# Optimization experiments

Hardware: AMD Instinct MI355X
Metric: run time of the kernel (lower is better)

Reference implementation:

```python
import jax, jax.numpy as jnp
import numpy as np

G = 32            # gridsize
N = G * G         # num_nodes = 1024
F_IN = 32         # input_dim
H = 256           # hidden_dim
L = 4             # n_layers
B = 64            # batch
MID = F_IN + L * H
MIN_VAL = -10000000.0
EPS_LN = 1e-5
EPS_BN = 1e-5


def _grid_edges():
    ids = np.arange(N).reshape(G, G)
    hs, hd = ids[:, :-1].ravel(), ids[:, 1:].ravel()
    vs, vd = ids[:-1, :].ravel(), ids[1:, :].ravel()
    src = np.concatenate([hs, hd, vs, vd]).astype(np.int32)
    dst = np.concatenate([hd, hs, vd, vs]).astype(np.int32)
    return jnp.asarray(src), jnp.asarray(dst)


def setup_inputs() -> dict:
    key = jax.random.key(0)
    ks = jax.random.split(key, 16)
    mask_f = jax.random.bernoulli(ks[0], 0.7, (B, N)).astype(jnp.float32)
    feats = jax.random.normal(ks[1], (B, N * F_IN), dtype=jnp.float32)
    observations = jnp.concatenate([mask_f, feats], axis=1)
    src, dst = _grid_edges()
    def lin(k, fi, fo):
        return jax.random.normal(k, (fi, fo), dtype=jnp.float32) / np.sqrt(fi)
    W0 = lin(ks[2], F_IN, H); b0 = jnp.zeros((H,), jnp.float32)
    g0 = jnp.ones((H,), jnp.float32); be0 = jnp.zeros((H,), jnp.float32)
    Ws = jax.random.normal(ks[3], (L - 1, H, H), jnp.float32) / np.sqrt(H)
    bs = jnp.zeros((L - 1, H), jnp.float32)
    gs = jnp.ones((L - 1, H), jnp.float32); bes = jnp.zeros((L - 1, H), jnp.float32)
    W1 = lin(ks[4], MID, 2 * H); b1 = jnp.zeros((2 * H,), jnp.float32)
    bn_g = jnp.ones((2 * H,), jnp.float32); bn_b = jnp.zeros((2 * H,), jnp.float32)
    bn_m = jax.random.normal(ks[5], (2 * H,), jnp.float32) * 0.1
    bn_v = jax.random.uniform(ks[6], (2 * H,), jnp.float32, 0.5, 1.5)
    W2 = lin(ks[7], 2 * H, 1); b2 = jnp.zeros((1,), jnp.float32)
    return {"observations": observations, "src": src, "dst": dst,
            "W0": W0, "b0": b0, "g0": g0, "be0": be0,
            "Ws": Ws, "bs": bs, "gs": gs, "bes": bes,
            "W1": W1, "b1": b1, "bn_g": bn_g, "bn_b": bn_b,
            "bn_m": bn_m, "bn_v": bn_v, "W2": W2, "b2": b2}


def _layer_norm(z, g, b):
    mu = z.mean(-1, keepdims=True)
    var = z.var(-1, keepdims=True)
    return (z - mu) / jnp.sqrt(var + EPS_LN) * g + b


def reference(observations, src, dst, W0, b0, g0, be0, Ws, bs, gs, bes,
              W1, b1, bn_g, bn_b, bn_m, bn_v, W2, b2):
    mask = observations[:, :N] != 0.0                      # [B,N] bool action mask
    x = observations[:, N:].reshape(B, N, F_IN)            # node features
    outs = [x]
    h = x
    for l in range(L):
        # GIN with eps=-1: (1+eps)*x_i vanishes -> mlp(sum of neighbor features)
        agg = jnp.zeros_like(h).at[:, dst, :].add(h[:, src, :])
        W, bb, g, be = ((W0, b0, g0, be0) if l == 0
                        else (Ws[l - 1], bs[l - 1], gs[l - 1], bes[l - 1]))
        h = jax.nn.relu(_layer_norm(agg @ W + bb, g, be))  # mlp ReLU; outer .relu() is idempotent
        outs.append(h)
    xc = jnp.concatenate(outs, axis=-1).reshape(B * N, MID)
    z = xc @ W1 + b1
    z = (z - bn_m) / jnp.sqrt(bn_v + EPS_BN) * bn_g + bn_b  # BatchNorm1d eval mode
    z = jax.nn.relu(z)                                       # dropout off in eval
    y = (z @ W2 + b2).reshape(B, N)
    return jnp.where(mask, y, MIN_VAL)
```

## Files before the change

### kernel.cpp

```cpp
#include <hip/hip_runtime.h>
#include <stdint.h>

#define FIN 32
#define HD 256
#define MIDK 1056
#define HF 512
#define MROWS 65536
#define OBS_STRIDE 33792

typedef float f32x2 __attribute__((ext_vector_type(2)));
typedef float f32x4 __attribute__((ext_vector_type(4)));

__device__ __forceinline__ unsigned pack4fp8(float a, float b, float c, float d) {
    int w = __builtin_amdgcn_cvt_pk_fp8_f32(a, b, 0, false);
    return (unsigned)__builtin_amdgcn_cvt_pk_fp8_f32(c, d, w, true);
}
__device__ __forceinline__ unsigned char f2fp8(float f) {
    return (unsigned char)(__builtin_amdgcn_cvt_pk_fp8_f32(f, f, 0, false) & 0xff);
}

__device__ __forceinline__ void glds16(const void* g, void* l) {
    __builtin_amdgcn_global_load_lds(
        (const __attribute__((address_space(1))) unsigned int*)g,
        (__attribute__((address_space(3))) unsigned int*)l,
        16, 0, 0);
}

__device__ __forceinline__ void gather16(const float* __restrict__ src, int stride, int n,
                                         unsigned char* __restrict__ dst) {
    float f[16];
#pragma unroll
    for (int j = 0; j < 16; ++j) f[j] = src[(size_t)j * stride + n];
    uint4 o;
    o.x = pack4fp8(f[0],  f[1],  f[2],  f[3]);
    o.y = pack4fp8(f[4],  f[5],  f[6],  f[7]);
    o.z = pack4fp8(f[8],  f[9],  f[10], f[11]);
    o.w = pack4fp8(f[12], f[13], f[14], f[15]);
    *(uint4*)dst = o;
}

__global__ __launch_bounds__(256) void k_prep_w(
        const float* __restrict__ W0, const float* __restrict__ Ws,
        const float* __restrict__ W1,
        unsigned char* __restrict__ Wt0, unsigned char* __restrict__ WtL,
        unsigned char* __restrict__ WtF) {
    const int b = blockIdx.x, t = threadIdx.x;
    if (b < 2) {
        int s = b * 256 + t;
        int hh = s >> 8, n = s & 255;
        gather16(W0 + (size_t)(hh * 16) * HD, HD, n, Wt0 + (size_t)s * 16);
    } else if (b < 50) {
        int u = (b - 2) * 256 + t;
        int l = u >> 12, s = u & 4095;
        int kb = s >> 9, hh = (s >> 8) & 1, n = s & 255;
        gather16(Ws + (size_t)l * 65536 + (size_t)(kb * 32 + hh * 16) * HD, HD, n,
                 WtL + (size_t)l * 65536 + (size_t)s * 16);
    } else {
        int s = (b - 50) * 256 + t;
        int kb = s >> 11, hh = (s >> 9) & 3, n = s & 511;
        int k0 = kb * 64 + hh * 16;
        if (k0 < MIDK)
            gather16(W1 + (size_t)k0 * HF, HF, n, WtF + (size_t)s * 16);
        else
            *(uint4*)(WtF + (size_t)s * 16) = make_uint4(0, 0, 0, 0);
    }
}

template <int K>
__global__ __launch_bounds__(256, 4) void k_layer(
        const unsigned char* __restrict__ Hin,
        const float* __restrict__ obs,
        const unsigned char* __restrict__ Wt,
        const float* __restrict__ bias, const float* __restrict__ gamma,
        const float* __restrict__ beta, unsigned char* __restrict__ Hout) {
    constexpr int KB = K / 32;
    __shared__ __align__(16) unsigned char Agg[(K / 16) * 64 * 16];
    __shared__ float ls[64], lss[64];
    const int t = threadIdx.x;
    const int w = t >> 6, lane = t & 63, quad = lane >> 4, l15 = lane & 15;
    const int q1 = quad >> 1, q0 = quad & 1;
    const int m0 = ((blockIdx.x & 7) * 128 + (blockIdx.x >> 3)) * 64;
    if (t < 64) { ls[t] = 0.f; lss[t] = 0.f; }

    if constexpr (K == 256) {
        const int r32 = t >> 3, seg = t & 7;
        const size_t rowBase = (size_t)(m0 & ~1023);
#pragma unroll
        for (int p = 0; p < 2; ++p) {
            const int r = p * 32 + r32;
            const int node = (m0 + r) & 1023;
            const int rr = node >> 5, cc = node & 31;
            float s[32];
#pragma unroll
            for (int i = 0; i < 32; ++i) s[i] = 0.f;
            auto addn = [&](int nn) {
                const uint4* pp = (const uint4*)(Hin + (rowBase + nn) * (size_t)K + seg * 32);
                uint4 u0 = pp[0], u1 = pp[1];
                unsigned uu[8] = {u0.x, u0.y, u0.z, u0.w, u1.x, u1.y, u1.z, u1.w};
#pragma unroll
                for (int i = 0; i < 8; ++i) {
                    f32x2 lo = __builtin_amdgcn_cvt_pk_f32_fp8(uu[i], false);
                    f32x2 hi = __builtin_amdgcn_cvt_pk_f32_fp8(uu[i], true);
                    s[4 * i + 0] += lo.x; s[4 * i + 1] += lo.y;
                    s[4 * i + 2] += hi.x; s[4 * i + 3] += hi.y;
                }
            };
            if (cc > 0)  addn(node - 1);
            if (cc < 31) addn(node + 1);
            if (rr > 0)  addn(node - 32);
            if (rr < 31) addn(node + 32);
            unsigned ow[8];
#pragma unroll
            for (int i = 0; i < 8; ++i)
                ow[i] = pack4fp8(s[4 * i], s[4 * i + 1], s[4 * i + 2], s[4 * i + 3]);
            ((uint4*)Agg)[(2 * seg) * 64 + r]     = make_uint4(ow[0], ow[1], ow[2], ow[3]);
            ((uint4*)Agg)[(2 * seg + 1) * 64 + r] = make_uint4(ow[4], ow[5], ow[6], ow[7]);
        }
    } else {
        const int r = t >> 2, seg4 = t & 3;
        const int bimg = m0 >> 10;
        const int node = (m0 + r) & 1023;
        const int rr = node >> 5, cc = node & 31;
        const float* fb = obs + (size_t)bimg * OBS_STRIDE + 1024 + seg4 * 8;
        float s[8] = {0, 0, 0, 0, 0, 0, 0, 0};
        auto addnf = [&](int nn) {
            const float4* fp = (const float4*)(fb + nn * 32);
            float4 f0 = fp[0], f1 = fp[1];
            s[0] += f0.x; s[1] += f0.y; s[2] += f0.z; s[3] += f0.w;
            s[4] += f1.x; s[5] += f1.y; s[6] += f1.z; s[7] += f1.w;
        };
        if (cc > 0)  addnf(node - 1);
        if (cc < 31) addnf(node + 1);
        if (rr > 0)  addnf(node - 32);
        if (rr < 31) addnf(node + 32);
        uint2 o;
        o.x = pack4fp8(s[0], s[1], s[2], s[3]);
        o.y = pack4fp8(s[4], s[5], s[6], s[7]);
        *(uint2*)(Agg + ((seg4 >> 1) * 64 + r) * 16 + (seg4 & 1) * 8) = o;
    }
    __syncthreads();

    f32x4 acc[4][4] = {};
    const unsigned char* bbase = Wt + ((size_t)(q1 * 256 + w * 64 + l15)) * 16 + q0 * 8;
    const unsigned char* abase = Agg + ((size_t)(q1 * 64 + l15)) * 16 + q0 * 8;

#define LOADBL(dst, kb) { const unsigned char* bp = bbase + (size_t)(kb) * 8192; \
    dst[0] = *(const long long*)(bp);        dst[1] = *(const long long*)(bp + 256); \
    dst[2] = *(const long long*)(bp + 512);  dst[3] = *(const long long*)(bp + 768); }
#define MFMAL(buf, kb) { long long af[4]; \
    _Pragma("unroll") for (int mt = 0; mt < 4; ++mt) \
        af[mt] = *(const long long*)(abase + (kb) * 2048 + mt * 256); \
    _Pragma("unroll") for (int mt = 0; mt < 4; ++mt) \
    _Pragma("unroll") for (int nt = 0; nt < 4; ++nt) \
        acc[mt][nt] = __builtin_amdgcn_mfma_f32_16x16x32_fp8_fp8(af[mt], buf[nt], acc[mt][nt], 0, 0, 0); }

    if constexpr (KB == 1) {
        long long bA[4];
        LOADBL(bA, 0);
        MFMAL(bA, 0);
    } else {
        long long bA[4], bB[4];
        LOADBL(bA, 0);
#pragma unroll
        for (int j = 0; j < KB / 2 - 1; ++j) {
            LOADBL(bB, 2 * j + 1);
            MFMAL(bA, 2 * j);
            LOADBL(bA, 2 * j + 2);
            MFMAL(bB, 2 * j + 1);
        }
        LOADBL(bB, KB - 1);
        MFMAL(bA, KB - 2);
        MFMAL(bB, KB - 1);
    }
#undef LOADBL
#undef MFMAL

#pragma unroll
    for (int mt = 0; mt < 4; ++mt) {
        float s0 = 0, s1 = 0, s2 = 0, s3 = 0, u0 = 0, u1 = 0, u2 = 0, u3 = 0;
#pragma unroll
        for (int nt = 0; nt < 4; ++nt) {
            int col = w * 64 + nt * 16 + l15;
            float bv = bias[col];
            f32x4 vv = acc[mt][nt];
            vv.x += bv; vv.y += bv; vv.z += bv; vv.w += bv;
            acc[mt][nt] = vv;
            s0 += vv.x; u0 += vv.x * vv.x;
            s1 += vv.y; u1 += vv.y * vv.y;
            s2 += vv.z; u2 += vv.z * vv.z;
            s3 += vv.w; u3 += vv.w * vv.w;
        }
#pragma unroll
        for (int msk = 1; msk < 16; msk <<= 1) {
            s0 += __shfl_xor(s0, msk); u0 += __shfl_xor(u0, msk);
            s1 += __shfl_xor(s1, msk); u1 += __shfl_xor(u1, msk);
            s2 += __shfl_xor(s2, msk); u2 += __shfl_xor(u2, msk);
            s3 += __shfl_xor(s3, msk); u3 += __shfl_xor(u3, msk);
        }
        if (l15 == 0) {
            int rl = mt * 16 + quad * 4;
            atomicAdd(&ls[rl + 0], s0); atomicAdd(&lss[rl + 0], u0);
            atomicAdd(&ls[rl + 1], s1); atomicAdd(&lss[rl + 1], u1);
            atomicAdd(&ls[rl + 2], s2); atomicAdd(&lss[rl + 2], u2);
            atomicAdd(&ls[rl + 3], s3); atomicAdd(&lss[rl + 3], u3);
        }
    }
    __syncthreads();
#pragma unroll
    for (int mt = 0; mt < 4; ++mt) {
        int rl = mt * 16 + quad * 4;
        float mu0 = ls[rl + 0] * (1.f / 256.f), mu1 = ls[rl + 1] * (1.f / 256.f);
        float mu2 = ls[rl + 2] * (1.f / 256.f), mu3 = ls[rl + 3] * (1.f / 256.f);
        float rs0 = rsqrtf(lss[rl + 0] * (1.f / 256.f) - mu0 * mu0 + 1e-5f);
        float rs1 = rsqrtf(lss[rl + 1] * (1.f / 256.f) - mu1 * mu1 + 1e-5f);
        float rs2 = rsqrtf(lss[rl + 2] * (1.f / 256.f) - mu2 * mu2 + 1e-5f);
        float rs3 = rsqrtf(lss[rl + 3] * (1.f / 256.f) - mu3 * mu3 + 1e-5f);
#pragma unroll
        for (int nt = 0; nt < 4; ++nt) {
            int col = w * 64 + nt * 16 + l15;
            float gg = gamma[col], be = beta[col];
            f32x4 vv = acc[mt][nt];
            size_t rb = (size_t)(m0 + mt * 16 + quad * 4) * HD + col;
            Hout[rb]          = f2fp8(fmaxf((vv.x - mu0) * rs0 * gg + be, 0.f));
            Hout[rb + HD]     = f2fp8(fmaxf((vv.y - mu1) * rs1 * gg + be, 0.f));
            Hout[rb + 2 * HD] = f2fp8(fmaxf((vv.z - mu2) * rs2 * gg + be, 0.f));
            Hout[rb + 3 * HD] = f2fp8(fmaxf((vv.w - mu3) * rs3 * gg + be, 0.f));
        }
    }
}

__global__ __launch_bounds__(512) void k_final(
        const unsigned char* __restrict__ h0, const unsigned char* __restrict__ h1,
        const unsigned char* __restrict__ h2, const unsigned char* __restrict__ h3,
        const unsigned char* __restrict__ WtF,
        const float* __restrict__ b1,
        const float* __restrict__ bng, const float* __restrict__ bnb,
        const float* __restrict__ bnm, const float* __restrict__ bnv,
        const float* __restrict__ W2, const float* __restrict__ b2,
        const float* __restrict__ obs, float* __restrict__ out) {
    __shared__ __align__(16) unsigned char As[264 * 16];
    __shared__ __align__(16) unsigned char Bsm[2056 * 16];
    __shared__ float yred[64];
    const int t = threadIdx.x;
    const int w = t >> 6, lane = t & 63, quad = lane >> 4, l15 = lane & 15;
    const int q1 = quad >> 1, q0 = quad & 1;
    const int wr = w >> 2, wc = w & 3;
    const int m0 = ((blockIdx.x & 7) * 128 + (blockIdx.x >> 3)) * 64;
    const int bimg = m0 >> 10, node0 = m0 & 1023;
    if (t < 64) yred[t] = 0.f;

    const unsigned char* hbuf[4] = {h0, h1, h2, h3};
    f32x4 acc[2][8] = {};

    for (int iter = 0; iter < 17; ++iter) {
        const int kb = iter * 64;
        const int steps = (iter < 16) ? 2 : 1;
        if (iter == 0) {
            if (t < 128) {
                int h = t >> 6, r = t & 63;
                const float* p = obs + (size_t)bimg * OBS_STRIDE + 1024 + (node0 + r) * 32 + h * 16;
                float4 f0 = *(const float4*)p, f1 = *(const float4*)(p + 4);
                float4 f2 = *(const float4*)(p + 8), f3 = *(const float4*)(p + 12);
                uint4 o;
                o.x = pack4fp8(f0.x, f0.y, f0.z, f0.w);
                o.y = pack4fp8(f1.x, f1.y, f1.z, f1.w);
                o.z = pack4fp8(f2.x, f2.y, f2.z, f2.w);
                o.w = pack4fp8(f3.x, f3.y, f3.z, f3.w);
                *(uint4*)(As + (h * 66 + r) * 16) = o;
            } else if (t < 256) {
                int h = t >> 6;
                glds16(h0 + (size_t)(m0 + (t & 63)) * HD + (h - 2) * 16,
                       As + (size_t)h * 66 * 16);
            }
        } else if (t < steps * 128) {
            int h = t >> 6, r = t & 63;
            int j = kb + h * 16 - FIN;
            glds16(hbuf[j >> 8] + (size_t)(m0 + r) * HD + (j & 255),
                   As + (size_t)h * 66 * 16);
        }
        for (int i = 0; i < steps * 2; ++i)
            glds16(WtF + ((size_t)iter * 2048 + i * 512 + t) * 16,
                   Bsm + ((size_t)i * 514 + (t & ~63)) * 16);
        __syncthreads();
#pragma unroll 2
        for (int s2 = 0; s2 < steps; ++s2) {
            long long af[2], bf[8];
#pragma unroll
            for (int mt = 0; mt < 2; ++mt)
                af[mt] = *(const long long*)(As + ((s2 * 2 + q1) * 66 + wr * 32 + mt * 16 + l15) * 16 + q0 * 8);
#pragma unroll
            for (int nt = 0; nt < 8; ++nt)
                bf[nt] = *(const long long*)(Bsm + ((size_t)((s2 * 2 + q1) * 514 + wc * 128 + nt * 16 + l15)) * 16 + q0 * 8);
#pragma unroll
            for (int mt = 0; mt < 2; ++mt)
#pragma unroll
                for (int nt = 0; nt < 8; ++nt)
                    acc[mt][nt] = __builtin_amdgcn_mfma_f32_16x16x32_fp8_fp8(af[mt], bf[nt], acc[mt][nt], 0, 0, 0);
        }
        __syncthreads();
    }

    float scv[8], sbv[8], w2v[8];
#pragma unroll
    for (int nt = 0; nt < 8; ++nt) {
        int col = wc * 128 + nt * 16 + l15;
        float sc = bng[col] * rsqrtf(bnv[col] + 1e-5f);
        scv[nt] = sc;
        sbv[nt] = (b1[col] - bnm[col]) * sc + bnb[col];
        w2v[nt] = W2[col];
    }
#pragma unroll
    for (int mt = 0; mt < 2; ++mt) {
        float p0 = 0, p1 = 0, p2 = 0, p3 = 0;
#pragma unroll
        for (int nt = 0; nt < 8; ++nt) {
            f32x4 vv = acc[mt][nt];
            p0 += fmaxf(vv.x * scv[nt] + sbv[nt], 0.f) * w2v[nt];
            p1 += fmaxf(vv.y * scv[nt] + sbv[nt], 0.f) * w2v[nt];
            p2 += fmaxf(vv.z * scv[nt] + sbv[nt], 0.f) * w2v[nt];
            p3 += fmaxf(vv.w * scv[nt] + sbv[nt], 0.f) * w2v[nt];
        }
#pragma unroll
        for (int msk = 1; msk < 16; msk <<= 1) {
            p0 += __shfl_xor(p0, msk);
            p1 += __shfl_xor(p1, msk);
            p2 += __shfl_xor(p2, msk);
            p3 += __shfl_xor(p3, msk);
        }
        if (l15 == 0) {
            int rl = wr * 32 + mt * 16 + quad * 4;
            atomicAdd(&yred[rl + 0], p0);
            atomicAdd(&yred[rl + 1], p1);
            atomicAdd(&yred[rl + 2], p2);
            atomicAdd(&yred[rl + 3], p3);
        }
    }
    __syncthreads();
    if (t < 64) {
        int gm = m0 + t;
        float mk = obs[(size_t)bimg * OBS_STRIDE + (node0 + t)];
        out[gm] = (mk != 0.f) ? yred[t] + b2[0] : -10000000.0f;
    }
}

extern "C" void kernel_launch(void* const* d_in, const int* in_sizes, int n_in,
                              void* d_out, int out_size, void* d_ws, size_t ws_size,
                              hipStream_t stream) {
    const float* obs = (const float*)d_in[0];
    const float* W0  = (const float*)d_in[3];
    const float* b0  = (const float*)d_in[4];
    const float* g0  = (const float*)d_in[5];
    const float* be0 = (const float*)d_in[6];
    const float* Ws  = (const float*)d_in[7];
    const float* bs  = (const float*)d_in[8];
    const float* gs  = (const float*)d_in[9];
    const float* bes = (const float*)d_in[10];
    const float* W1  = (const float*)d_in[11];
    const float* b1  = (const float*)d_in[12];
    const float* bng = (const float*)d_in[13];
    const float* bnb = (const float*)d_in[14];
    const float* bnm = (const float*)d_in[15];
    const float* bnv = (const float*)d_in[16];
    const float* W2  = (const float*)d_in[17];
    const float* b2  = (const float*)d_in[18];
    float* out = (float*)d_out;

    char* ws = (char*)d_ws;
    unsigned char* h0  = (unsigned char*)(ws);
    unsigned char* h1  = (unsigned char*)(ws + 16777216);
    unsigned char* h2  = (unsigned char*)(ws + 33554432);
    unsigned char* h3  = (unsigned char*)(ws + 50331648);
    unsigned char* Wt0 = (unsigned char*)(ws + 67108864);
    unsigned char* WtL = (unsigned char*)(ws + 67117056);
    unsigned char* WtF = (unsigned char*)(ws + 67313664);

    k_prep_w<<<182, 256, 0, stream>>>(W0, Ws, W1, Wt0, WtL, WtF);

    k_layer<FIN><<<1024, 256, 0, stream>>>(h0 , obs, Wt0, b0, g0, be0, h0);
    k_layer<HD> <<<1024, 256, 0, stream>>>(h0, obs, WtL,              bs,       gs,       bes,       h1);
    k_layer<HD> <<<1024, 256, 0, stream>>>(h1, obs, WtL + 65536,      bs + 256, gs + 256, bes + 256, h2);
    k_layer<HD> <<<1024, 256, 0, stream>>>(h2, obs, WtL + 2 * 65536,  bs + 512, gs + 512, bes + 512, h3);

    k_final<<<1024, 512, 0, stream>>>(h0, h1, h2, h3, WtF, b1, bng, bnb, bnm, bnv,
                                      W2, b2, obs, out);
}
```

Baseline: 242.3 us.

## Give each wave its own 16 rows and all 256 columns in GIN layer kernel

The GIN layer kernel is restructured so each wave owns 16 output rows across the full 256-column width, instead of all four waves sharing 64 rows and splitting the columns. Each wave now aggregates its own rows into a private LDS region, so both __syncthreads barriers and the shared-memory atomic LayerNorm reduction are gone; row statistics finish with in-wave shuffles only. The trade-off is that every wave now reads the entire weight matrix rather than a quarter of it, which raises global/L2 traffic for B, and each wave holds 16 accumulators plus 16 buffered B fragments in registers.

```diff
diff --git a/kernel.cpp b/kernel.cpp
--- a/kernel.cpp
+++ b/kernel.cpp
@@ -74,158 +74,126 @@
         const float* __restrict__ bias, const float* __restrict__ gamma,
         const float* __restrict__ beta, unsigned char* __restrict__ Hout) {
     constexpr int KB = K / 32;
-    __shared__ __align__(16) unsigned char Agg[(K / 16) * 64 * 16];
-    __shared__ float ls[64], lss[64];
+    __shared__ __align__(16) unsigned char Agg[4 * (K / 16) * 16 * 16];
     const int t = threadIdx.x;
     const int w = t >> 6, lane = t & 63, quad = lane >> 4, l15 = lane & 15;
     const int q1 = quad >> 1, q0 = quad & 1;
     const int m0 = ((blockIdx.x & 7) * 128 + (blockIdx.x >> 3)) * 64;
-    if (t < 64) { ls[t] = 0.f; lss[t] = 0.f; }
-
-    if constexpr (K == 256) {
-        const int r32 = t >> 3, seg = t & 7;
-        const size_t rowBase = (size_t)(m0 & ~1023);
-#pragma unroll
-        for (int p = 0; p < 2; ++p) {
-            const int r = p * 32 + r32;
-            const int node = (m0 + r) & 1023;
-            const int rr = node >> 5, cc = node & 31;
-            float s[32];
-#pragma unroll
-            for (int i = 0; i < 32; ++i) s[i] = 0.f;
-            auto addn = [&](int nn) {
-                const uint4* pp = (const uint4*)(Hin + (rowBase + nn) * (size_t)K + seg * 32);
-                uint4 u0 = pp[0], u1 = pp[1];
-                unsigned uu[8] = {u0.x, u0.y, u0.z, u0.w, u1.x, u1.y, u1.z, u1.w};
-#pragma unroll
-                for (int i = 0; i < 8; ++i) {
-                    f32x2 lo = __builtin_amdgcn_cvt_pk_f32_fp8(uu[i], false);
-                    f32x2 hi = __builtin_amdgcn_cvt_pk_f32_fp8(uu[i], true);
-                    s[4 * i + 0] += lo.x; s[4 * i + 1] += lo.y;
-                    s[4 * i + 2] += hi.x; s[4 * i + 3] += hi.y;
-                }
+    const int wm0 = m0 + w * 16;
+    const int wunit = w * (K / 16) * 16;
+
+    {
+        const int r = lane & 15, rep = lane >> 4;
+        const int gm = wm0 + r;
+        const int node = gm & 1023;
+        const int rr = node >> 5, cc = node & 31;
+        if constexpr (K == 256) {
+            const size_t rowBase = (size_t)(gm & ~1023) * K;
+#pragma unroll
+            for (int sp = 0; sp < 2; ++sp) {
+                const int k0 = rep * 64 + sp * 32;
+                f32x2 s[16] = {};
+                auto addn = [&](int nn) {
+                    const uint4* p = (const uint4*)(Hin + rowBase + (size_t)nn * K + k0);
+                    uint4 u0 = p[0], u1 = p[1];
+                    unsigned uu[8] = {u0.x, u0.y, u0.z, u0.w, u1.x, u1.y, u1.z, u1.w};
+#pragma unroll
+                    for (int i = 0; i < 8; ++i) {
+                        s[2 * i]     += __builtin_amdgcn_cvt_pk_f32_fp8(uu[i], false);
+                        s[2 * i + 1] += __builtin_amdgcn_cvt_pk_f32_fp8(uu[i], true);
+                    }
+                };
+                if (cc > 0)  addn(node - 1);
+                if (cc < 31) addn(node + 1);
+                if (rr > 0)  addn(node - 32);
+                if (rr < 31) addn(node + 32);
+                unsigned ow[8];
+#pragma unroll
+                for (int i = 0; i < 8; ++i)
+                    ow[i] = pack4fp8(s[2 * i].x, s[2 * i].y, s[2 * i + 1].x, s[2 * i + 1].y);
+                const int h = k0 >> 4;
+                ((uint4*)Agg)[wunit + h * 16 + r]       = make_uint4(ow[0], ow[1], ow[2], ow[3]);
+                ((uint4*)Agg)[wunit + (h + 1) * 16 + r] = make_uint4(ow[4], ow[5], ow[6], ow[7]);
+            }
+        } else {
+            const int bimg = wm0 >> 10;
+            const float* fb = obs + (size_t)bimg * OBS_STRIDE + 1024 + rep * 8;
+            float s[8] = {0, 0, 0, 0, 0, 0, 0, 0};
+            auto addnf = [&](int nn) {
+                const float4* fp = (const float4*)(fb + nn * 32);
+                float4 f0 = fp[0], f1 = fp[1];
+                s[0] += f0.x; s[1] += f0.y; s[2] += f0.z; s[3] += f0.w;
+                s[4] += f1.x; s[5] += f1.y; s[6] += f1.z; s[7] += f1.w;
             };
-            if (cc > 0)  addn(node - 1);
-            if (cc < 31) addn(node + 1);
-            if (rr > 0)  addn(node - 32);
-            if (rr < 31) addn(node + 32);
-            unsigned ow[8];
-#pragma unroll
-            for (int i = 0; i < 8; ++i)
-                ow[i] = pack4fp8(s[4 * i], s[4 * i + 1], s[4 * i + 2], s[4 * i + 3]);
-            ((uint4*)Agg)[(2 * seg) * 64 + r]     = make_uint4(ow[0], ow[1], ow[2], ow[3]);
-            ((uint4*)Agg)[(2 * seg + 1) * 64 + r] = make_uint4(ow[4], ow[5], ow[6], ow[7]);
-        }
-    } else {
-        const int r = t >> 2, seg4 = t & 3;
-        const int bimg = m0 >> 10;
-        const int node = (m0 + r) & 1023;
-        const int rr = node >> 5, cc = node & 31;
-        const float* fb = obs + (size_t)bimg * OBS_STRIDE + 1024 + seg4 * 8;
-        float s[8] = {0, 0, 0, 0, 0, 0, 0, 0};
-        auto addnf = [&](int nn) {
-            const float4* fp = (const float4*)(fb + nn * 32);
-            float4 f0 = fp[0], f1 = fp[1];
-            s[0] += f0.x; s[1] += f0.y; s[2] += f0.z; s[3] += f0.w;
-            s[4] += f1.x; s[5] += f1.y; s[6] += f1.z; s[7] += f1.w;
-        };
-        if (cc > 0)  addnf(node - 1);
-        if (cc < 31) addnf(node + 1);
-        if (rr > 0)  addnf(node - 32);
-        if (rr < 31) addnf(node + 32);
-        uint2 o;
-        o.x = pack4fp8(s[0], s[1], s[2], s[3]);
-        o.y = pack4fp8(s[4], s[5], s[6], s[7]);
-        *(uint2*)(Agg + ((seg4 >> 1) * 64 + r) * 16 + (seg4 & 1) * 8) = o;
-    }
-    __syncthreads();
-
-    f32x4 acc[4][4] = {};
-    const unsigned char* bbase = Wt + ((size_t)(q1 * 256 + w * 64 + l15)) * 16 + q0 * 8;
-    const unsigned char* abase = Agg + ((size_t)(q1 * 64 + l15)) * 16 + q0 * 8;
-
-#define LOADBL(dst, kb) { const unsigned char* bp = bbase + (size_t)(kb) * 8192; \
-    dst[0] = *(const long long*)(bp);        dst[1] = *(const long long*)(bp + 256); \
-    dst[2] = *(const long long*)(bp + 512);  dst[3] = *(const long long*)(bp + 768); }
-#define MFMAL(buf, kb) { long long af[4]; \
-    _Pragma("unroll") for (int mt = 0; mt < 4; ++mt) \
-        af[mt] = *(const long long*)(abase + (kb) * 2048 + mt * 256); \
-    _Pragma("unroll") for (int mt = 0; mt < 4; ++mt) \
-    _Pragma("unroll") for (int nt = 0; nt < 4; ++nt) \
-        acc[mt][nt] = __builtin_amdgcn_mfma_f32_16x16x32_fp8_fp8(af[mt], buf[nt], acc[mt][nt], 0, 0, 0); }
-
-    if constexpr (KB == 1) {
-        long long bA[4];
-        LOADBL(bA, 0);
-        MFMAL(bA, 0);
-    } else {
-        long long bA[4], bB[4];
-        LOADBL(bA, 0);
-#pragma unroll
-        for (int j = 0; j < KB / 2 - 1; ++j) {
-            LOADBL(bB, 2 * j + 1);
-            MFMAL(bA, 2 * j);
-            LOADBL(bA, 2 * j + 2);
-            MFMAL(bB, 2 * j + 1);
-        }
-        LOADBL(bB, KB - 1);
-        MFMAL(bA, KB - 2);
-        MFMAL(bB, KB - 1);
-    }
-#undef LOADBL
-#undef MFMAL
-
-#pragma unroll
-    for (int mt = 0; mt < 4; ++mt) {
-        float s0 = 0, s1 = 0, s2 = 0, s3 = 0, u0 = 0, u1 = 0, u2 = 0, u3 = 0;
-#pragma unroll
-        for (int nt = 0; nt < 4; ++nt) {
-            int col = w * 64 + nt * 16 + l15;
-            float bv = bias[col];
-            f32x4 vv = acc[mt][nt];
-            vv.x += bv; vv.y += bv; vv.z += bv; vv.w += bv;
-            acc[mt][nt] = vv;
-            s0 += vv.x; u0 += vv.x * vv.x;
-            s1 += vv.y; u1 += vv.y * vv.y;
-            s2 += vv.z; u2 += vv.z * vv.z;
-            s3 += vv.w; u3 += vv.w * vv.w;
-        }
-#pragma unroll
-        for (int msk = 1; msk < 16; msk <<= 1) {
-            s0 += __shfl_xor(s0, msk); u0 += __shfl_xor(u0, msk);
-            s1 += __shfl_xor(s1, msk); u1 += __shfl_xor(u1, msk);
-            s2 += __shfl_xor(s2, msk); u2 += __shfl_xor(u2, msk);
-            s3 += __shfl_xor(s3, msk); u3 += __shfl_xor(u3, msk);
-        }
-        if (l15 == 0) {
-            int rl = mt * 16 + quad * 4;
-            atomicAdd(&ls[rl + 0], s0); atomicAdd(&lss[rl + 0], u0);
-            atomicAdd(&ls[rl + 1], s1); atomicAdd(&lss[rl + 1], u1);
-            atomicAdd(&ls[rl + 2], s2); atomicAdd(&lss[rl + 2], u2);
-            atomicAdd(&ls[rl + 3], s3); atomicAdd(&lss[rl + 3], u3);
-        }
-    }
-    __syncthreads();
-#pragma unroll
-    for (int mt = 0; mt < 4; ++mt) {
-        int rl = mt * 16 + quad * 4;
-        float mu0 = ls[rl + 0] * (1.f / 256.f), mu1 = ls[rl + 1] * (1.f / 256.f);
-        float mu2 = ls[rl + 2] * (1.f / 256.f), mu3 = ls[rl + 3] * (1.f / 256.f);
-        float rs0 = rsqrtf(lss[rl + 0] * (1.f / 256.f) - mu0 * mu0 + 1e-5f);
-        float rs1 = rsqrtf(lss[rl + 1] * (1.f / 256.f) - mu1 * mu1 + 1e-5f);
-        float rs2 = rsqrtf(lss[rl + 2] * (1.f / 256.f) - mu2 * mu2 + 1e-5f);
-        float rs3 = rsqrtf(lss[rl + 3] * (1.f / 256.f) - mu3 * mu3 + 1e-5f);
-#pragma unroll
-        for (int nt = 0; nt < 4; ++nt) {
-            int col = w * 64 + nt * 16 + l15;
-            float gg = gamma[col], be = beta[col];
-            f32x4 vv = acc[mt][nt];
-            size_t rb = (size_t)(m0 + mt * 16 + quad * 4) * HD + col;
-            Hout[rb]          = f2fp8(fmaxf((vv.x - mu0) * rs0 * gg + be, 0.f));
-            Hout[rb + HD]     = f2fp8(fmaxf((vv.y - mu1) * rs1 * gg + be, 0.f));
-            Hout[rb + 2 * HD] = f2fp8(fmaxf((vv.z - mu2) * rs2 * gg + be, 0.f));
-            Hout[rb + 3 * HD] = f2fp8(fmaxf((vv.w - mu3) * rs3 * gg + be, 0.f));
-        }
+            if (cc > 0)  addnf(node - 1);
+            if (cc < 31) addnf(node + 1);
+            if (rr > 0)  addnf(node - 32);
+            if (rr < 31) addnf(node + 32);
+            uint2 o;
+            o.x = pack4fp8(s[0], s[1], s[2], s[3]);
+            o.y = pack4fp8(s[4], s[5], s[6], s[7]);
+            *(uint2*)(Agg + (size_t)(wunit + (rep >> 1) * 16 + r) * 16 + (rep & 1) * 8) = o;
+        }
+    }
+
+    f32x4 acc[16] = {};
+    const unsigned char* bbase = Wt + ((size_t)(q1 * 256 + l15)) * 16 + q0 * 8;
+    const unsigned char* abase = Agg + (size_t)(wunit + q1 * 16 + l15) * 16 + q0 * 8;
+
+    long long gA[8], gB[8];
+#define LOADH(dst, c, half) { const unsigned char* bp = bbase + (size_t)(c) * 8192 + (half) * 2048; \
+    _Pragma("unroll") for (int j = 0; j < 8; ++j) dst[j] = *(const long long*)(bp + j * 256); }
+#define MFMAH(buf, c, half) { \
+    long long af = *(const long long*)(abase + (size_t)(c) * 512); \
+    _Pragma("unroll") for (int j = 0; j < 8; ++j) \
+        acc[(half) * 8 + j] = __builtin_amdgcn_mfma_f32_16x16x32_fp8_fp8(af, buf[j], acc[(half) * 8 + j], 0, 0, 0); }
+
+    LOADH(gA, 0, 0);
+#pragma unroll
+    for (int c = 0; c < KB; ++c) {
+        LOADH(gB, c, 1);
+        MFMAH(gA, c, 0);
+        if (c + 1 < KB) LOADH(gA, c + 1, 0);
+        MFMAH(gB, c, 1);
+    }
+#undef LOADH
+#undef MFMAH
+
+    float s0 = 0, s1 = 0, s2 = 0, s3 = 0, u0 = 0, u1 = 0, u2 = 0, u3 = 0;
+#pragma unroll
+    for (int nt = 0; nt < 16; ++nt) {
+        float bv = bias[nt * 16 + l15];
+        f32x4 vv = acc[nt];
+        vv.x += bv; vv.y += bv; vv.z += bv; vv.w += bv;
+        acc[nt] = vv;
+        s0 += vv.x; u0 += vv.x * vv.x;
+        s1 += vv.y; u1 += vv.y * vv.y;
+        s2 += vv.z; u2 += vv.z * vv.z;
+        s3 += vv.w; u3 += vv.w * vv.w;
+    }
+#pragma unroll
+    for (int msk = 1; msk < 16; msk <<= 1) {
+        s0 += __shfl_xor(s0, msk); u0 += __shfl_xor(u0, msk);
+        s1 += __shfl_xor(s1, msk); u1 += __shfl_xor(u1, msk);
+        s2 += __shfl_xor(s2, msk); u2 += __shfl_xor(u2, msk);
+        s3 += __shfl_xor(s3, msk); u3 += __shfl_xor(u3, msk);
+    }
+    const float mu0 = s0 * (1.f / 256.f), mu1 = s1 * (1.f / 256.f);
+    const float mu2 = s2 * (1.f / 256.f), mu3 = s3 * (1.f / 256.f);
+    const float rs0 = rsqrtf(u0 * (1.f / 256.f) - mu0 * mu0 + 1e-5f);
+    const float rs1 = rsqrtf(u1 * (1.f / 256.f) - mu1 * mu1 + 1e-5f);
+    const float rs2 = rsqrtf(u2 * (1.f / 256.f) - mu2 * mu2 + 1e-5f);
+    const float rs3 = rsqrtf(u3 * (1.f / 256.f) - mu3 * mu3 + 1e-5f);
+#pragma unroll
+    for (int nt = 0; nt < 16; ++nt) {
+        int col = nt * 16 + l15;
+        float gg = gamma[col], be = beta[col];
+        f32x4 vv = acc[nt];
+        size_t rb = (size_t)(wm0 + quad * 4) * HD + col;
+        Hout[rb]          = f2fp8(fmaxf((vv.x - mu0) * rs0 * gg + be, 0.f));
+        Hout[rb + HD]     = f2fp8(fmaxf((vv.y - mu1) * rs1 * gg + be, 0.f));
+        Hout[rb + 2 * HD] = f2fp8(fmaxf((vv.z - mu2) * rs2 * gg + be, 0.f));
+        Hout[rb + 3 * HD] = f2fp8(fmaxf((vv.w - mu3) * rs3 * gg + be, 0.f));
     }
 }
 
```

After: 327.6 us. 35.2% more time.

## Stage layer weights through double-buffered LDS via async global-to-LDS loads

Applied to the files above, without the earlier changes.

The GIN layer GEMM used to load its fp8 weight fragments straight from global memory into registers with a manual register double-buffer. It now copies each 32-wide K slab of weights into a two-slot LDS buffer with global_load_lds, prefetching the next slab while the MFMAs run on the current one. This aims to replace many small 8-byte global loads with coalesced 16-byte async copies shared across the four waves. In exchange it adds 16KB of LDS, which may lower occupancy under launch_bounds(256,4), and a __syncthreads per K step.

```diff
diff --git a/kernel.cpp b/kernel.cpp
--- a/kernel.cpp
+++ b/kernel.cpp
@@ -75,12 +75,19 @@
         const float* __restrict__ beta, unsigned char* __restrict__ Hout) {
     constexpr int KB = K / 32;
     __shared__ __align__(16) unsigned char Agg[(K / 16) * 64 * 16];
+    __shared__ __align__(16) unsigned char Bs[2][512 * 16];
     __shared__ float ls[64], lss[64];
     const int t = threadIdx.x;
     const int w = t >> 6, lane = t & 63, quad = lane >> 4, l15 = lane & 15;
     const int q1 = quad >> 1, q0 = quad & 1;
     const int m0 = ((blockIdx.x & 7) * 128 + (blockIdx.x >> 3)) * 64;
     if (t < 64) { ls[t] = 0.f; lss[t] = 0.f; }
+
+#pragma unroll
+    for (int i = 0; i < 2; ++i) {
+        int s = i * 256 + t;
+        glds16(Wt + (size_t)s * 16, Bs[0] + (size_t)(s & ~63) * 16);
+    }
 
     if constexpr (K == 256) {
         const int r32 = t >> 3, seg = t & 7;
@@ -141,39 +148,31 @@
     __syncthreads();
 
     f32x4 acc[4][4] = {};
-    const unsigned char* bbase = Wt + ((size_t)(q1 * 256 + w * 64 + l15)) * 16 + q0 * 8;
-    const unsigned char* abase = Agg + ((size_t)(q1 * 64 + l15)) * 16 + q0 * 8;
-
-#define LOADBL(dst, kb) { const unsigned char* bp = bbase + (size_t)(kb) * 8192; \
-    dst[0] = *(const long long*)(bp);        dst[1] = *(const long long*)(bp + 256); \
-    dst[2] = *(const long long*)(bp + 512);  dst[3] = *(const long long*)(bp + 768); }
-#define MFMAL(buf, kb) { long long af[4]; \
-    _Pragma("unroll") for (int mt = 0; mt < 4; ++mt) \
-        af[mt] = *(const long long*)(abase + (kb) * 2048 + mt * 256); \
-    _Pragma("unroll") for (int mt = 0; mt < 4; ++mt) \
-    _Pragma("unroll") for (int nt = 0; nt < 4; ++nt) \
-        acc[mt][nt] = __builtin_amdgcn_mfma_f32_16x16x32_fp8_fp8(af[mt], buf[nt], acc[mt][nt], 0, 0, 0); }
-
-    if constexpr (KB == 1) {
-        long long bA[4];
-        LOADBL(bA, 0);
-        MFMAL(bA, 0);
-    } else {
-        long long bA[4], bB[4];
-        LOADBL(bA, 0);
-#pragma unroll
-        for (int j = 0; j < KB / 2 - 1; ++j) {
-            LOADBL(bB, 2 * j + 1);
-            MFMAL(bA, 2 * j);
-            LOADBL(bA, 2 * j + 2);
-            MFMAL(bB, 2 * j + 1);
-        }
-        LOADBL(bB, KB - 1);
-        MFMAL(bA, KB - 2);
-        MFMAL(bB, KB - 1);
-    }
-#undef LOADBL
-#undef MFMAL
+#pragma unroll
+    for (int kb = 0; kb < KB; ++kb) {
+        if (kb + 1 < KB) {
+#pragma unroll
+            for (int i = 0; i < 2; ++i) {
+                int s = i * 256 + t;
+                glds16(Wt + ((size_t)(kb + 1) * 512 + s) * 16,
+                       Bs[(kb + 1) & 1] + (size_t)(s & ~63) * 16);
+            }
+        }
+        const unsigned char* bbuf = Bs[kb & 1];
+        long long af[4], bf[4];
+#pragma unroll
+        for (int nt = 0; nt < 4; ++nt)
+            bf[nt] = *(const long long*)(bbuf + ((size_t)(q1 * 256 + w * 64 + nt * 16 + l15)) * 16 + q0 * 8);
+#pragma unroll
+        for (int mt = 0; mt < 4; ++mt)
+            af[mt] = *(const long long*)(Agg + ((2 * kb + q1) * 64 + mt * 16 + l15) * 16 + q0 * 8);
+#pragma unroll
+        for (int mt = 0; mt < 4; ++mt)
+#pragma unroll
+            for (int nt = 0; nt < 4; ++nt)
+                acc[mt][nt] = __builtin_amdgcn_mfma_f32_16x16x32_fp8_fp8(af[mt], bf[nt], acc[mt][nt], 0, 0, 0);
+        __syncthreads();
+    }
 
 #pragma unroll
     for (int mt = 0; mt < 4; ++mt) {
```

Result: slower. 252.8 us (+4.4%).

## Store hidden activations in 16-byte k-chunk-major layout per image

Applied to the files above, without the earlier changes.

Changes the intermediate fp8 hidden buffers from row-major [node][256] to a blocked layout [image][k-chunk of 16][node][16 bytes]. Neighbor gathers, the epilogue stores and the final kernel's global-to-LDS loads are all rewritten for this layout, so adjacent lanes touch contiguous 16-byte chunks and the loads coalesce better. The gather thread mapping also changes so that a wavefront covers 64 consecutive nodes for one segment. The cost is that the epilogue still writes single bytes, now with a stride of 16 bytes between rows, which may hurt write coalescing.

```diff
diff --git a/kernel.cpp b/kernel.cpp
--- a/kernel.cpp
+++ b/kernel.cpp
@@ -10,6 +10,7 @@
 
 typedef float f32x2 __attribute__((ext_vector_type(2)));
 typedef float f32x4 __attribute__((ext_vector_type(4)));
+
 
 __device__ __forceinline__ unsigned pack4fp8(float a, float b, float c, float d) {
     int w = __builtin_amdgcn_cvt_pk_fp8_f32(a, b, 0, false);
@@ -80,22 +81,23 @@
     const int w = t >> 6, lane = t & 63, quad = lane >> 4, l15 = lane & 15;
     const int q1 = quad >> 1, q0 = quad & 1;
     const int m0 = ((blockIdx.x & 7) * 128 + (blockIdx.x >> 3)) * 64;
+    const int img = m0 >> 10, node0 = m0 & 1023;
     if (t < 64) { ls[t] = 0.f; lss[t] = 0.f; }
 
     if constexpr (K == 256) {
-        const int r32 = t >> 3, seg = t & 7;
-        const size_t rowBase = (size_t)(m0 & ~1023);
+        const int r = t & 63, sg = t >> 6;
+        const int node = node0 + r;
+        const int rr = node >> 5, cc = node & 31;
+        const unsigned char* Hb = Hin + (size_t)img * 262144;
 #pragma unroll
         for (int p = 0; p < 2; ++p) {
-            const int r = p * 32 + r32;
-            const int node = (m0 + r) & 1023;
-            const int rr = node >> 5, cc = node & 31;
+            const int seg = p * 4 + sg;
             float s[32];
 #pragma unroll
             for (int i = 0; i < 32; ++i) s[i] = 0.f;
             auto addn = [&](int nn) {
-                const uint4* pp = (const uint4*)(Hin + (rowBase + nn) * (size_t)K + seg * 32);
-                uint4 u0 = pp[0], u1 = pp[1];
+                uint4 u0 = *(const uint4*)(Hb + ((size_t)(2 * seg) * 1024 + nn) * 16);
+                uint4 u1 = *(const uint4*)(Hb + ((size_t)(2 * seg + 1) * 1024 + nn) * 16);
                 unsigned uu[8] = {u0.x, u0.y, u0.z, u0.w, u1.x, u1.y, u1.z, u1.w};
 #pragma unroll
                 for (int i = 0; i < 8; ++i) {
@@ -118,10 +120,9 @@
         }
     } else {
         const int r = t >> 2, seg4 = t & 3;
-        const int bimg = m0 >> 10;
-        const int node = (m0 + r) & 1023;
+        const int node = node0 + r;
         const int rr = node >> 5, cc = node & 31;
-        const float* fb = obs + (size_t)bimg * OBS_STRIDE + 1024 + seg4 * 8;
+        const float* fb = obs + (size_t)img * OBS_STRIDE + 1024 + seg4 * 8;
         float s[8] = {0, 0, 0, 0, 0, 0, 0, 0};
         auto addnf = [&](int nn) {
             const float4* fp = (const float4*)(fb + nn * 32);
@@ -220,11 +221,12 @@
             int col = w * 64 + nt * 16 + l15;
             float gg = gamma[col], be = beta[col];
             f32x4 vv = acc[mt][nt];
-            size_t rb = (size_t)(m0 + mt * 16 + quad * 4) * HD + col;
-            Hout[rb]          = f2fp8(fmaxf((vv.x - mu0) * rs0 * gg + be, 0.f));
-            Hout[rb + HD]     = f2fp8(fmaxf((vv.y - mu1) * rs1 * gg + be, 0.f));
-            Hout[rb + 2 * HD] = f2fp8(fmaxf((vv.z - mu2) * rs2 * gg + be, 0.f));
-            Hout[rb + 3 * HD] = f2fp8(fmaxf((vv.w - mu3) * rs3 * gg + be, 0.f));
+            size_t rb = ((size_t)(img * 16 + w * 4 + nt) * 1024
+                         + node0 + mt * 16 + quad * 4) * 16 + l15;
+            Hout[rb]      = f2fp8(fmaxf((vv.x - mu0) * rs0 * gg + be, 0.f));
+            Hout[rb + 16] = f2fp8(fmaxf((vv.y - mu1) * rs1 * gg + be, 0.f));
+            Hout[rb + 32] = f2fp8(fmaxf((vv.z - mu2) * rs2 * gg + be, 0.f));
+            Hout[rb + 48] = f2fp8(fmaxf((vv.w - mu3) * rs3 * gg + be, 0.f));
         }
     }
 }
@@ -268,14 +270,14 @@
                 o.w = pack4fp8(f3.x, f3.y, f3.z, f3.w);
                 *(uint4*)(As + (h * 66 + r) * 16) = o;
             } else if (t < 256) {
-                int h = t >> 6;
-                glds16(h0 + (size_t)(m0 + (t & 63)) * HD + (h - 2) * 16,
+                int h = t >> 6, r = t & 63;
+                glds16(h0 + ((size_t)(bimg * 16 + (h - 2)) * 1024 + node0 + r) * 16,
                        As + (size_t)h * 66 * 16);
             }
         } else if (t < steps * 128) {
             int h = t >> 6, r = t & 63;
             int j = kb + h * 16 - FIN;
-            glds16(hbuf[j >> 8] + (size_t)(m0 + r) * HD + (j & 255),
+            glds16(hbuf[j >> 8] + ((size_t)(bimg * 16 + ((j & 255) >> 4)) * 1024 + node0 + r) * 16,
                    As + (size_t)h * 66 * 16);
         }
         for (int i = 0; i < steps * 2; ++i)
```

Result: faster. 234.1 us (-3.4%).
